# Performance work log

Measured on AMD Instinct MI355X. Metric: run time of the kernel, lower is better.

## Reference

```python
import jax, jax.numpy as jnp
import numpy as np

STATE_DIM = 13
HIDDEN = 1024
NUM_SENSORS = 32
BATCH = 131072


def _sensor_locations():
    # Replicates the torch buffer construction (linspace over theta/phi on a sphere of radius 2)
    sensor_range = 2.0
    theta = np.linspace(0.0, 2.0 * np.pi, NUM_SENSORS // 2, dtype=np.float64)
    phi = np.linspace(0.0, np.pi, 2, dtype=np.float64)
    sensors = []
    for p in phi:
        for t in theta:
            sensors.append([sensor_range * np.sin(p) * np.cos(t),
                            sensor_range * np.sin(p) * np.sin(t),
                            sensor_range * np.cos(p)])
    return jnp.asarray(np.asarray(sensors[:NUM_SENSORS], dtype=np.float32))


def setup_inputs() -> dict:
    key = jax.random.key(0)
    ks = jax.random.split(key, 24)

    def lin(kw, fan_in, fan_out):
        # torch nn.Linear default init: U(-1/sqrt(fan_in), 1/sqrt(fan_in))
        bound = 1.0 / np.sqrt(fan_in)
        w = jax.random.uniform(kw, (fan_in, fan_out), jnp.float32, -bound, bound)
        return w

    def bias(kb, fan_in, fan_out):
        bound = 1.0 / np.sqrt(fan_in)
        return jax.random.uniform(kb, (fan_out,), jnp.float32, -bound, bound)

    branch_in = NUM_SENSORS * (STATE_DIM + 4)  # 544
    h2, h4, h8 = HIDDEN // 2, HIDDEN // 4, HIDDEN // 8
    inp = {
        "state": jax.random.normal(ks[0], (BATCH, STATE_DIM), jnp.float32),
        "action": jax.random.normal(ks[1], (BATCH, 4), jnp.float32),
        "sensor_locations": _sensor_locations(),
        "bw1": lin(ks[2], branch_in, HIDDEN), "bb1": bias(ks[3], branch_in, HIDDEN),
        "bw2": lin(ks[4], HIDDEN, h2), "bb2": bias(ks[5], HIDDEN, h2),
        "bw3": lin(ks[6], h2, h4), "bb3": bias(ks[7], h2, h4),
        "tw1": lin(ks[8], 3, h4), "tb1": bias(ks[9], 3, h4),
        "tw2": lin(ks[10], h4, h4), "tb2": bias(ks[11], h4, h4),
        "qw1": lin(ks[12], 3, h8), "qb1": bias(ks[13], 3, h8),
        "qw2": lin(ks[14], h8, STATE_DIM), "qb2": bias(ks[15], h8, STATE_DIM),
        "pw": lin(ks[16], h4, STATE_DIM), "pb": bias(ks[17], h4, STATE_DIM),
        "residual_weight": jnp.float32(0.1),
    }
    return inp


def reference(state, action, sensor_locations,
              bw1, bb1, bw2, bb2, bw3, bb3,
              tw1, tb1, tw2, tb2,
              qw1, qb1, qw2, qb2,
              pw, pb, residual_weight):
    B = state.shape[0]
    pos = state[:, :3]

    # Vectorized sensor encoding (replaces the 32-iteration python loop):
    # distance [B, S, 1], weight = exp(-d/0.5)
    diff = sensor_locations[None, :, :] - pos[:, None, :]          # [B, S, 3]
    dist = jnp.linalg.norm(diff, axis=-1, keepdims=True)           # [B, S, 1]
    w = jnp.exp(-dist / 0.5)                                       # [B, S, 1]
    sv = jnp.concatenate([state[:, None, :] * w,
                          action[:, None, :] * w], axis=-1)        # [B, S, sd+4]
    enc = sv.reshape(B, -1)                                        # [B, S*(sd+4)]

    # Branch net (dropout is identity in eval mode)
    h = jax.nn.relu(enc @ bw1 + bb1)
    h = jax.nn.relu(h @ bw2 + bb2)
    branch = h @ bw3 + bb3                                         # [B, hidden//4]

    # Trunk net on eval coords
    t = jnp.tanh(pos @ tw1 + tb1)
    trunk = jnp.tanh(t @ tw2 + tb2)                                # [B, hidden//4]

    interaction = branch * trunk
    output_delta = interaction @ pw + pb                           # [B, state_dim]

    b = jax.nn.relu(pos @ qw1 + qb1)
    bias_out = b @ qw2 + qb2                                       # [B, state_dim]

    next_state = state + residual_weight * (output_delta + bias_out)

    # Quaternion normalization for dims 3:7 (state_dim >= 7)
    quat = next_state[:, 3:7]
    qn = jnp.linalg.norm(quat, axis=1, keepdims=True)
    next_state = next_state.at[:, 3:7].set(quat / (qn + 1e-8))
    return next_state
```

## Files before the change

kernel.cpp:

```cpp
#include <hip/hip_runtime.h>
#include <hip/hip_bf16.h>
#include <hip/hip_fp8.h>

#define B_TOTAL 131072

typedef __attribute__((ext_vector_type(8))) short short8;
typedef __attribute__((ext_vector_type(4))) float f32x4;
typedef __attribute__((ext_vector_type(16))) unsigned char uchar16;
typedef unsigned int uint;

#define MFMA(a,b,c) __builtin_amdgcn_mfma_f32_16x16x32_bf16(a,b,c,0,0,0)
#define MFMA8(a,b,c) __builtin_amdgcn_mfma_f32_16x16x32_fp8_fp8(a,b,c,0,0,0)

__device__ __forceinline__ short f2bf(float f) {
  union { float f; uint u; } x; x.f = f;
  uint r = x.u + 0x7fffu + ((x.u >> 16) & 1u);
  return (short)(r >> 16);
}
__device__ __forceinline__ unsigned char f2fp8(float v) {
  union { __hip_fp8_e4m3 q; unsigned char b; } u;
  u.q = __hip_fp8_e4m3(v);
  return u.b;
}
__device__ __forceinline__ float ftanh(float x) {
  float e = __builtin_amdgcn_exp2f(x * 2.8853900817779268f);
  return 1.f - 2.f * __builtin_amdgcn_rcpf(e + 1.f);
}

__device__ __forceinline__ void gl_lds16(const void* g, void* l) {
  __builtin_amdgcn_global_load_lds((const __attribute__((address_space(1))) uint*)g,
                                   (__attribute__((address_space(3))) uint*)l, 16, 0, 0);
}
__device__ __forceinline__ int swz8(int c, int r) { return (c & ~7) | ((c ^ r) & 7); }

__global__ __launch_bounds__(256)
void prep(const float* __restrict__ bw1, const float* __restrict__ bw2,
          const float* __restrict__ bw3, const float* __restrict__ tw2,
          const float* __restrict__ pw, const float* __restrict__ qw2,
          unsigned char* __restrict__ w1f, unsigned char* __restrict__ w2f,
          unsigned char* __restrict__ w3r, short* __restrict__ w4r,
          short* __restrict__ pwT, short* __restrict__ qw2T) {
  __shared__ float tile[32][33];
  int b = blockIdx.x;
  if (b == 1280) {
    for (int t = threadIdx.x; t < 6144; t += 256) {
      if (t < 4096) { int c = t >> 8, k = t & 255;
        pwT[t] = (c < 13) ? f2bf(pw[k * 13 + c]) : (short)0; }
      else { int i = t - 4096; int c = i >> 7, j = i & 127;
        qw2T[i] = (c < 13) ? f2bf(qw2[j * 13 + c]) : (short)0; }
    }
    return;
  }
  const float* src; int K, N, mat;
  if (b < 576)       { src = bw1; K = 544;  N = 1024; mat = 0; }
  else if (b < 1088) { b -= 576;  src = bw2; K = 1024; N = 512;  mat = 1; }
  else if (b < 1216) { b -= 1088; src = bw3; K = 512;  N = 256;  mat = 2; }
  else               { b -= 1216; src = tw2; K = 256;  N = 256;  mat = 3; }
  const int ntk = (mat == 0) ? 18 : (mat == 1) ? 32 : (mat == 2) ? 16 : 8;
  const int tn = b / ntk, tk = b % ntk;
  const int k0 = tk * 32, n0 = tn * 32;
  const int tx = threadIdx.x & 31, ty = threadIdx.x >> 5;
#pragma unroll
  for (int rr = 0; rr < 32; rr += 8) {
    int k = k0 + ty + rr;
    tile[ty + rr][tx] = (k < K) ? src[(long)k * N + n0 + tx] : 0.f;
  }
  __syncthreads();
#pragma unroll
  for (int rr = 0; rr < 32; rr += 8) {
    int nl = ty + rr;
    int n = n0 + nl, k = k0 + tx;
    float v = tile[tx][nl];
    if (mat == 0) w1f[(long)n * 576 + k] = f2fp8(v);
    else if (mat == 1) w2f[(long)n * 1024 + k] = f2fp8(v);
    else {
      int ks = k >> 5, fq = (k >> 3) & 3, j = k & 7;
      int wb = n >> 5, hf = (n >> 4) & 1, fr = n & 15;
      long idx = (long)(((ks * 8 + wb) * 2 + hf) * 4 + fq) * 128 + fr * 8 + j;
      if (mat == 2) w3r[idx] = f2fp8(v);
      else          w4r[idx] = f2bf(v);
    }
  }
}

__global__ __launch_bounds__(256)
void enc_k(const float* __restrict__ state, const float* __restrict__ action,
           const float* __restrict__ sensors, unsigned char* __restrict__ enc) {
  __shared__ float sval[64][17];
  __shared__ float wexp[64][32];
  __shared__ float sens[96];
  const int tid = threadIdx.x;
  const int rb = blockIdx.x * 64;
  if (tid < 96) sens[tid] = sensors[tid];
  for (int i = tid; i < 64 * 17; i += 256) {
    const int r = i / 17, c = i % 17;
    const long grow = rb + r;
    sval[r][c] = (c < 13) ? state[grow * 13 + c] : action[grow * 4 + (c - 13)];
  }
  __syncthreads();
  for (int i = tid; i < 64 * 32; i += 256) {
    const int r = i >> 5, s = i & 31;
    const float dx = sens[s*3+0] - sval[r][0];
    const float dy = sens[s*3+1] - sval[r][1];
    const float dz = sens[s*3+2] - sval[r][2];
    wexp[r][s] = __expf(-2.0f * sqrtf(dx*dx + dy*dy + dz*dz));
  }
  __syncthreads();
  for (int i = tid; i < 64 * 36; i += 256) {
    const int r = i / 36, c16 = i % 36;
    uchar16 v;
#pragma unroll
    for (int j = 0; j < 16; ++j) {
      const int k = c16 * 16 + j;
      unsigned char o = 0;
      if (k < 544) { const int s = k / 17, c = k % 17; o = f2fp8(sval[r][c] * wexp[r][s]); }
      v[j] = o;
    }
    *(uchar16*)&enc[((long)(rb + r)) * 576 + c16 * 16] = v;
  }
}

template<int N, int K, int ACT>
__global__ __launch_bounds__(256, 4)
void gemm_f8(const unsigned char* __restrict__ A, const unsigned char* __restrict__ Bt,
             const float* __restrict__ bias, unsigned char* __restrict__ C) {
  constexpr int NT = K / 64;
  constexpr int NTN = N / 128;
  __shared__ __align__(16) unsigned char As[2][128 * 64];
  __shared__ __align__(16) unsigned char Bs[2][128 * 64];
  const int tid = threadIdx.x;
  const int wave = tid >> 6;
  const int lane = tid & 63;
  const int Mtiles = gridDim.x / NTN;
  const int bid = blockIdx.x;
  const int xcd = bid & 7, seq = bid >> 3;
  const int tm = xcd * (Mtiles >> 3) + seq / NTN;
  const int tn = seq % NTN;
  const long arow0 = (long)tm * 128;
  const long brow0 = (long)tn * 128;

  auto stage = [&](int b, int kt) {
    const int k0 = kt * 64;
#pragma unroll
    for (int it = 0; it < 2; ++it) {
      const int ch = it * 256 + tid;
      const int row = ch >> 2;
      const int cs = (ch & 3) ^ ((row >> 1) & 3);
      gl_lds16(A + (arow0 + row) * (long)K + k0 + cs * 16, &As[b][ch * 16]);
      gl_lds16(Bt + (brow0 + row) * (long)K + k0 + cs * 16, &Bs[b][ch * 16]);
    }
  };

  const int wr = (wave >> 1) * 64;
  const int wc = (wave & 1) * 64;
  const int fr = lane & 15;
  const int fg = lane >> 4;

  f32x4 acc[4][4] = {};

  stage(0, 0);
  for (int kt = 0; kt < NT; ++kt) {
    const int cur = kt & 1;
    __syncthreads();
    if (kt + 1 < NT) stage(cur ^ 1, kt + 1);
    const unsigned char* Ab = As[cur];
    const unsigned char* Bb = Bs[cur];
    long long af[4][2], bfr[4][2];
#pragma unroll
    for (int m = 0; m < 4; ++m)
#pragma unroll
      for (int kk = 0; kk < 2; ++kk) {
        const int row = wr + m * 16 + fr;
        const int c16 = (kk * 2 + (fg >> 1)) ^ ((row >> 1) & 3);
        af[m][kk] = *(const long long*)&Ab[row * 64 + c16 * 16 + (fg & 1) * 8];
      }
#pragma unroll
    for (int n = 0; n < 4; ++n)
#pragma unroll
      for (int kk = 0; kk < 2; ++kk) {
        const int col = wc + n * 16 + fr;
        const int c16 = (kk * 2 + (fg >> 1)) ^ ((col >> 1) & 3);
        bfr[n][kk] = *(const long long*)&Bb[col * 64 + c16 * 16 + (fg & 1) * 8];
      }
#pragma unroll
    for (int kk = 0; kk < 2; ++kk)
#pragma unroll
      for (int m = 0; m < 4; ++m)
#pragma unroll
        for (int n = 0; n < 4; ++n)
          acc[m][n] = MFMA8(af[m][kk], bfr[n][kk], acc[m][n]);
  }

  float bv[4];
#pragma unroll
  for (int n = 0; n < 4; ++n) bv[n] = bias[tn * 128 + wc + n * 16 + fr];
#pragma unroll
  for (int m = 0; m < 4; ++m)
#pragma unroll
    for (int n = 0; n < 4; ++n) {
      const long col = brow0 + wc + n * 16 + fr;
#pragma unroll
      for (int r = 0; r < 4; ++r) {
        const long row = arow0 + wr + m * 16 + fg * 4 + r;
        float v = acc[m][n][r] + bv[n];
        if (ACT == 1) v = fmaxf(v, 0.f);
        C[row * (long)N + col] = f2fp8(v);
      }
    }
}

__global__ __launch_bounds__(512)
void k2(const unsigned char* __restrict__ h2, const float* __restrict__ state,
        const float* __restrict__ tw1, const float* __restrict__ tb1,
        const unsigned char* __restrict__ w3r, const float* __restrict__ bb3,
        const short* __restrict__ w4r, const float* __restrict__ tb2,
        const short* __restrict__ pwT, const float* __restrict__ qw1,
        const short* __restrict__ qw2T, const float* __restrict__ qb1,
        const float* __restrict__ pb, const float* __restrict__ qb2,
        const float* __restrict__ rwp, float* __restrict__ out) {
  __shared__ __align__(16) char lds[77824];
  char*  h2S = lds;
  short* tS  = (short*)(lds + 32768);
  short* pwS = (short*)(lds + 65536);
  short* q2S = (short*)(lds + 73728);
  short* hqS = (short*)lds;
  float* prS = (float*)(lds + 16384);
  float* pr2S= (float*)(lds + 20480);

  const int tid = threadIdx.x, wave = tid >> 6, lane = tid & 63;
  const int fr = lane & 15, fg = lane >> 4;
  const long rb = (long)blockIdx.x * 64;

  long long b3r[16][2];
#pragma unroll
  for (int ks = 0; ks < 16; ++ks) {
    b3r[ks][0] = *(const long long*)&w3r[(long)((ks * 8 + wave) * 2 + 0) * 512 + lane * 8];
    b3r[ks][1] = *(const long long*)&w3r[(long)((ks * 8 + wave) * 2 + 1) * 512 + lane * 8];
  }
#pragma unroll
  for (int it = 0; it < 4; ++it) {
    int ch = it * 512 + tid;
    int row = ch >> 5, c = ch & 31;
    gl_lds16(h2 + (rb + row) * 512 + ((c ^ (row & 7)) << 4), h2S + ch * 16);
  }
  { int row = tid >> 5, c = tid & 31;
    gl_lds16(pwT + (long)row * 256 + swz8(c, row) * 8, (char*)pwS + tid * 16); }
  if (tid < 256) { int row = tid >> 4, c = tid & 15;
    gl_lds16(qw2T + (long)row * 128 + swz8(c, row) * 8, (char*)q2S + tid * 16); }
  short8 b4r[8][2];
#pragma unroll
  for (int ks = 0; ks < 8; ++ks) {
    b4r[ks][0] = *(const short8*)&w4r[(long)((ks * 8 + wave) * 2 + 0) * 512 + lane * 8];
    b4r[ks][1] = *(const short8*)&w4r[(long)((ks * 8 + wave) * 2 + 1) * 512 + lane * 8];
  }

  for (int i = tid; i < 64 * 32; i += 512) {
    int r = i >> 5, c8 = i & 31;
    float p0 = state[(rb + r) * 13 + 0], p1 = state[(rb + r) * 13 + 1], p2 = state[(rb + r) * 13 + 2];
    short8 v;
#pragma unroll
    for (int j = 0; j < 8; ++j) {
      int jj = c8 * 8 + j;
      v[j] = f2bf(ftanh(p0 * tw1[jj] + p1 * tw1[256 + jj] + p2 * tw1[512 + jj] + tb1[jj]));
    }
    *(short8*)&tS[(r * 32 + swz8(c8, r)) * 8] = v;
  }
  __syncthreads();

  f32x4 acc3[4][2] = {};
#pragma unroll
  for (int ks = 0; ks < 16; ++ks) {
    long long a[4];
#pragma unroll
    for (int mf = 0; mf < 4; ++mf) {
      int row = mf * 16 + fr;
      int c16 = (ks * 2 + (fg >> 1)) ^ (row & 7);
      a[mf] = *(const long long*)&h2S[row * 512 + c16 * 16 + ((fg & 1) << 3)];
    }
#pragma unroll
    for (int mf = 0; mf < 4; ++mf) {
      acc3[mf][0] = MFMA8(a[mf], b3r[ks][0], acc3[mf][0]);
      acc3[mf][1] = MFMA8(a[mf], b3r[ks][1], acc3[mf][1]);
    }
  }

  f32x4 accT[4][2] = {};
#pragma unroll
  for (int ks = 0; ks < 8; ++ks) {
#pragma unroll
    for (int mf = 0; mf < 4; ++mf) {
      int row = mf * 16 + fr;
      short8 aF = *(const short8*)&tS[row * 256 + swz8(ks * 4 + fg, row) * 8];
      accT[mf][0] = MFMA(aF, b4r[ks][0], accT[mf][0]);
      accT[mf][1] = MFMA(aF, b4r[ks][1], accT[mf][1]);
    }
  }
  __syncthreads();

#pragma unroll
  for (int nf = 0; nf < 2; ++nf) {
    int col = wave * 32 + nf * 16 + fr;
    float b3 = bb3[col], t2 = tb2[col];
#pragma unroll
    for (int mf = 0; mf < 4; ++mf)
#pragma unroll
      for (int i = 0; i < 4; ++i) {
        int row = mf * 16 + fg * 4 + i;
        float br = acc3[mf][nf][i] + b3;
        float tr = ftanh(accT[mf][nf][i] + t2);
        tS[row * 256 + swz8(col >> 3, row) * 8 + (col & 7)] = f2bf(br * tr);
      }
  }
  {
    int r = tid >> 3, j0 = (tid & 7) * 16;
    float p0 = state[(rb + r) * 13 + 0], p1 = state[(rb + r) * 13 + 1], p2 = state[(rb + r) * 13 + 2];
#pragma unroll
    for (int cc = 0; cc < 2; ++cc) {
      short8 v;
#pragma unroll
      for (int j = 0; j < 8; ++j) {
        int jj = j0 + cc * 8 + j;
        float hv = fmaxf(p0 * qw1[jj] + p1 * qw1[128 + jj] + p2 * qw1[256 + jj] + qb1[jj], 0.f);
        v[j] = f2bf(hv);
      }
      *(short8*)&hqS[(r * 16 + swz8(j0 / 8 + cc, r)) * 8] = v;
    }
  }
  __syncthreads();

  if (wave < 4) {
    int row = wave * 16 + fr;
    f32x4 accP = {0.f, 0.f, 0.f, 0.f};
#pragma unroll
    for (int ks = 0; ks < 8; ++ks) {
      short8 a = *(const short8*)&tS[row * 256 + swz8(ks * 4 + fg, row) * 8];
      short8 b = *(const short8*)&pwS[fr * 256 + swz8(ks * 4 + fg, fr) * 8];
      accP = MFMA(a, b, accP);
    }
#pragma unroll
    for (int i = 0; i < 4; ++i)
      prS[(wave * 16 + fg * 4 + i) * 16 + fr] = accP[i];
  } else {
    int row = (wave - 4) * 16 + fr;
    f32x4 accQ = {0.f, 0.f, 0.f, 0.f};
#pragma unroll
    for (int ks = 0; ks < 4; ++ks) {
      short8 a = *(const short8*)&hqS[row * 128 + swz8(ks * 4 + fg, row) * 8];
      short8 b = *(const short8*)&q2S[fr * 128 + swz8(ks * 4 + fg, fr) * 8];
      accQ = MFMA(a, b, accQ);
    }
#pragma unroll
    for (int i = 0; i < 4; ++i)
      pr2S[((wave - 4) * 16 + fg * 4 + i) * 16 + fr] = accQ[i];
  }
  __syncthreads();

  if (tid < 64) {
    int r = tid;
    float rw = rwp[0];
    float ns[13];
#pragma unroll
    for (int c = 0; c < 13; ++c)
      ns[c] = state[(rb + r) * 13 + c] + rw * (prS[r * 16 + c] + pr2S[r * 16 + c] + pb[c] + qb2[c]);
    float qn = sqrtf(ns[3] * ns[3] + ns[4] * ns[4] + ns[5] * ns[5] + ns[6] * ns[6]) + 1e-8f;
#pragma unroll
    for (int c = 3; c < 7; ++c) ns[c] /= qn;
#pragma unroll
    for (int c = 0; c < 13; ++c) out[(rb + r) * 13 + c] = ns[c];
  }
}

extern "C" void kernel_launch(void* const* d_in, const int* in_sizes, int n_in,
                              void* d_out, int out_size, void* d_ws, size_t ws_size,
                              hipStream_t stream) {
  const float* state  = (const float*)d_in[0];
  const float* action = (const float*)d_in[1];
  const float* sensors= (const float*)d_in[2];
  const float* bw1 = (const float*)d_in[3];
  const float* bb1 = (const float*)d_in[4];
  const float* bw2 = (const float*)d_in[5];
  const float* bb2 = (const float*)d_in[6];
  const float* bw3 = (const float*)d_in[7];
  const float* bb3 = (const float*)d_in[8];
  const float* tw1 = (const float*)d_in[9];
  const float* tb1 = (const float*)d_in[10];
  const float* tw2 = (const float*)d_in[11];
  const float* tb2 = (const float*)d_in[12];
  const float* qw1 = (const float*)d_in[13];
  const float* qb1 = (const float*)d_in[14];
  const float* qw2 = (const float*)d_in[15];
  const float* qb2 = (const float*)d_in[16];
  const float* pw  = (const float*)d_in[17];
  const float* pb  = (const float*)d_in[18];
  const float* rw  = (const float*)d_in[19];
  float* out = (float*)d_out;

  char* p = (char*)d_ws;
  unsigned char* w1f = (unsigned char*)p; p += (size_t)1024 * 576;
  unsigned char* w2f = (unsigned char*)p; p += (size_t)512 * 1024;
  unsigned char* w3r = (unsigned char*)p; p += (size_t)256 * 512;
  short* w4r = (short*)p;          p += (size_t)256 * 256 * 2;
  short* pwT = (short*)p;          p += (size_t)16 * 256 * 2;
  short* qw2T= (short*)p;          p += (size_t)16 * 128 * 2;
  const size_t fixed = (size_t)(p - (char*)d_ws);
  const size_t avail = (ws_size > fixed) ? ws_size - fixed : 0;
  long Mc = (long)(avail / 1600) & ~1023L;
  if (Mc > B_TOTAL) Mc = B_TOTAL;
  if (Mc < 1024) return;
  unsigned char* encb = (unsigned char*)p;
  unsigned char* h2b  = (unsigned char*)p;
  unsigned char* h1f  = (unsigned char*)(p + (size_t)Mc * 576);

  prep<<<dim3(1281), dim3(256), 0, stream>>>(bw1, bw2, bw3, tw2, pw, qw2,
                                             w1f, w2f, w3r, w4r, pwT, qw2T);

  for (long r0 = 0; r0 < B_TOTAL; r0 += Mc) {
    long Mr = B_TOTAL - r0; if (Mr > Mc) Mr = Mc;
    enc_k<<<dim3(Mr / 64), dim3(256), 0, stream>>>(state + r0 * 13, action + r0 * 4,
                                                   sensors, encb);
    gemm_f8<1024, 576, 1><<<dim3((Mr / 128) * 8), dim3(256), 0, stream>>>(
        encb, w1f, bb1, h1f);
    gemm_f8<512, 1024, 1><<<dim3((Mr / 128) * 4), dim3(256), 0, stream>>>(
        h1f, w2f, bb2, h2b);
    k2<<<dim3(Mr / 64), dim3(512), 0, stream>>>(h2b, state + r0 * 13, tw1, tb1,
                                                w3r, bb3, w4r, tb2, pwT, qw1, qw2T,
                                                qb1, pb, qb2, rw, out + r0 * 13);
  }
}
```

Measured before the change: 376.1 us.

## Permute K layout so fp8 GEMM fragments load as single 16-byte LDS reads

Reorders the K dimension of the encoded input, the fp8 weight matrices and the intermediate activations with a fixed permutation. Each lane can then fetch both K-halves of its MFMA fragment with one 128-bit LDS load instead of two 64-bit loads. The GEMM epilogue writes permuted columns, and the downstream k2 reader is adjusted to match. This cuts the number of LDS read instructions in the inner loop, at the cost of a more intricate layout contract shared by several kernels.

```diff
diff --git a/kernel.cpp b/kernel.cpp
--- a/kernel.cpp
+++ b/kernel.cpp
@@ -7,6 +7,7 @@
 typedef __attribute__((ext_vector_type(8))) short short8;
 typedef __attribute__((ext_vector_type(4))) float f32x4;
 typedef __attribute__((ext_vector_type(16))) unsigned char uchar16;
+typedef __attribute__((ext_vector_type(2))) long long llong2;
 typedef unsigned int uint;
 
 #define MFMA(a,b,c) __builtin_amdgcn_mfma_f32_16x16x32_bf16(a,b,c,0,0,0)
@@ -32,6 +33,10 @@
                                    (__attribute__((address_space(3))) uint*)l, 16, 0, 0);
 }
 __device__ __forceinline__ int swz8(int c, int r) { return (c & ~7) | ((c ^ r) & 7); }
+
+__device__ __forceinline__ int permk(int k) {
+  return (k & ~63) | (((k >> 3) & 3) << 4) | (((k >> 5) & 1) << 3) | (k & 7);
+}
 
 __global__ __launch_bounds__(256)
 void prep(const float* __restrict__ bw1, const float* __restrict__ bw2,
@@ -71,8 +76,8 @@
     int nl = ty + rr;
     int n = n0 + nl, k = k0 + tx;
     float v = tile[tx][nl];
-    if (mat == 0) w1f[(long)n * 576 + k] = f2fp8(v);
-    else if (mat == 1) w2f[(long)n * 1024 + k] = f2fp8(v);
+    if (mat == 0) w1f[(long)n * 576 + permk(k)] = f2fp8(v);
+    else if (mat == 1) w2f[(long)n * 1024 + permk(k)] = f2fp8(v);
     else {
       int ks = k >> 5, fq = (k >> 3) & 3, j = k & 7;
       int wb = n >> 5, hf = (n >> 4) & 1, fr = n & 15;
@@ -110,11 +115,13 @@
     const int r = i / 36, c16 = i % 36;
     uchar16 v;
 #pragma unroll
-    for (int j = 0; j < 16; ++j) {
-      const int k = c16 * 16 + j;
+    for (int j2 = 0; j2 < 16; ++j2) {
+      const int soff = c16 * 16 + j2;
+      const int kb = soff >> 6, bb = soff & 63;
+      const int k = kb * 64 + ((bb >> 3) & 1) * 32 + (bb >> 4) * 8 + (bb & 7);
       unsigned char o = 0;
       if (k < 544) { const int s = k / 17, c = k % 17; o = f2fp8(sval[r][c] * wexp[r][s]); }
-      v[j] = o;
+      v[j2] = o;
     }
     *(uchar16*)&enc[((long)(rb + r)) * 576 + c16 * 16] = v;
   }
@@ -165,30 +172,27 @@
     if (kt + 1 < NT) stage(cur ^ 1, kt + 1);
     const unsigned char* Ab = As[cur];
     const unsigned char* Bb = Bs[cur];
-    long long af[4][2], bfr[4][2];
+    llong2 av[4], bv2[4];
+#pragma unroll
+    for (int m = 0; m < 4; ++m) {
+      const int row = wr + m * 16 + fr;
+      av[m] = *(const llong2*)&Ab[row * 64 + ((fg ^ ((row >> 1) & 3)) << 4)];
+    }
+#pragma unroll
+    for (int n = 0; n < 4; ++n) {
+      const int col = wc + n * 16 + fr;
+      bv2[n] = *(const llong2*)&Bb[col * 64 + ((fg ^ ((col >> 1) & 3)) << 4)];
+    }
 #pragma unroll
     for (int m = 0; m < 4; ++m)
 #pragma unroll
-      for (int kk = 0; kk < 2; ++kk) {
-        const int row = wr + m * 16 + fr;
-        const int c16 = (kk * 2 + (fg >> 1)) ^ ((row >> 1) & 3);
-        af[m][kk] = *(const long long*)&Ab[row * 64 + c16 * 16 + (fg & 1) * 8];
-      }
-#pragma unroll
-    for (int n = 0; n < 4; ++n)
-#pragma unroll
-      for (int kk = 0; kk < 2; ++kk) {
-        const int col = wc + n * 16 + fr;
-        const int c16 = (kk * 2 + (fg >> 1)) ^ ((col >> 1) & 3);
-        bfr[n][kk] = *(const long long*)&Bb[col * 64 + c16 * 16 + (fg & 1) * 8];
-      }
-#pragma unroll
-    for (int kk = 0; kk < 2; ++kk)
-#pragma unroll
-      for (int m = 0; m < 4; ++m)
-#pragma unroll
-        for (int n = 0; n < 4; ++n)
-          acc[m][n] = MFMA8(af[m][kk], bfr[n][kk], acc[m][n]);
+      for (int n = 0; n < 4; ++n)
+        acc[m][n] = MFMA8(av[m][0], bv2[n][0], acc[m][n]);
+#pragma unroll
+    for (int m = 0; m < 4; ++m)
+#pragma unroll
+      for (int n = 0; n < 4; ++n)
+        acc[m][n] = MFMA8(av[m][1], bv2[n][1], acc[m][n]);
   }
 
   float bv[4];
@@ -198,7 +202,8 @@
   for (int m = 0; m < 4; ++m)
 #pragma unroll
     for (int n = 0; n < 4; ++n) {
-      const long col = brow0 + wc + n * 16 + fr;
+      const int colp = permk(tn * 128 + wc + n * 16 + fr);
+      const long col = (long)colp;
 #pragma unroll
       for (int r = 0; r < 4; ++r) {
         const long row = arow0 + wr + m * 16 + fg * 4 + r;
@@ -274,8 +279,8 @@
 #pragma unroll
     for (int mf = 0; mf < 4; ++mf) {
       int row = mf * 16 + fr;
-      int c16 = (ks * 2 + (fg >> 1)) ^ (row & 7);
-      a[mf] = *(const long long*)&h2S[row * 512 + c16 * 16 + ((fg & 1) << 3)];
+      int c16 = ((ks >> 1) * 4 + fg) ^ (row & 7);
+      a[mf] = *(const long long*)&h2S[row * 512 + (c16 << 4) + ((ks & 1) << 3)];
     }
 #pragma unroll
     for (int mf = 0; mf < 4; ++mf) {
```

New measurement: 381.8 us. About the same (+1.5%).

## Switch branch GEMMs to scaled 16x16x128 FP8 MFMA with K-tile 128

Applied to the files above, without the earlier changes.

Replaces the two fp8 branch-net GEMMs' 16x16x32 MFMAs with the MX scaled 16x16x128 f8f6f4 instruction using unit scales, doubling the LDS K-tile to 128 with a new 8-way swizzle. The first layer's K is padded from 576 to 640 so it divides by 128, which changes the encoder and weight-prep layouts and the workspace sizing. The aim is fewer MFMA issues and higher matrix throughput. In exchange, LDS use doubles, occupancy is lowered to 2 blocks per CU, and layer 1 does extra padded work.

```diff
diff --git a/kernel.cpp b/kernel.cpp
--- a/kernel.cpp
+++ b/kernel.cpp
@@ -7,10 +7,16 @@
 typedef __attribute__((ext_vector_type(8))) short short8;
 typedef __attribute__((ext_vector_type(4))) float f32x4;
 typedef __attribute__((ext_vector_type(16))) unsigned char uchar16;
+typedef __attribute__((ext_vector_type(4))) int int4v;
+typedef __attribute__((ext_vector_type(8))) int int8v;
 typedef unsigned int uint;
 
 #define MFMA(a,b,c) __builtin_amdgcn_mfma_f32_16x16x32_bf16(a,b,c,0,0,0)
 #define MFMA8(a,b,c) __builtin_amdgcn_mfma_f32_16x16x32_fp8_fp8(a,b,c,0,0,0)
+#define MFMAS(a,b,c) __builtin_amdgcn_mfma_scale_f32_16x16x128_f8f6f4( \
+    a, b, c, 0, 0, 0, 0x7F7F7F7F, 0, 0x7F7F7F7F)
+
+union V8U { int8v v; int4v h[2]; };
 
 __device__ __forceinline__ short f2bf(float f) {
   union { float f; uint u; } x; x.f = f;
@@ -42,7 +48,7 @@
           short* __restrict__ pwT, short* __restrict__ qw2T) {
   __shared__ float tile[32][33];
   int b = blockIdx.x;
-  if (b == 1280) {
+  if (b == 1344) {
     for (int t = threadIdx.x; t < 6144; t += 256) {
       if (t < 4096) { int c = t >> 8, k = t & 255;
         pwT[t] = (c < 13) ? f2bf(pw[k * 13 + c]) : (short)0; }
@@ -52,11 +58,11 @@
     return;
   }
   const float* src; int K, N, mat;
-  if (b < 576)       { src = bw1; K = 544;  N = 1024; mat = 0; }
-  else if (b < 1088) { b -= 576;  src = bw2; K = 1024; N = 512;  mat = 1; }
-  else if (b < 1216) { b -= 1088; src = bw3; K = 512;  N = 256;  mat = 2; }
-  else               { b -= 1216; src = tw2; K = 256;  N = 256;  mat = 3; }
-  const int ntk = (mat == 0) ? 18 : (mat == 1) ? 32 : (mat == 2) ? 16 : 8;
+  if (b < 640)       { src = bw1; K = 544;  N = 1024; mat = 0; }
+  else if (b < 1152) { b -= 640;  src = bw2; K = 1024; N = 512;  mat = 1; }
+  else if (b < 1280) { b -= 1152; src = bw3; K = 512;  N = 256;  mat = 2; }
+  else               { b -= 1280; src = tw2; K = 256;  N = 256;  mat = 3; }
+  const int ntk = (mat == 0) ? 20 : (mat == 1) ? 32 : (mat == 2) ? 16 : 8;
   const int tn = b / ntk, tk = b % ntk;
   const int k0 = tk * 32, n0 = tn * 32;
   const int tx = threadIdx.x & 31, ty = threadIdx.x >> 5;
@@ -71,7 +77,7 @@
     int nl = ty + rr;
     int n = n0 + nl, k = k0 + tx;
     float v = tile[tx][nl];
-    if (mat == 0) w1f[(long)n * 576 + k] = f2fp8(v);
+    if (mat == 0) w1f[(long)n * 640 + k] = f2fp8(v);
     else if (mat == 1) w2f[(long)n * 1024 + k] = f2fp8(v);
     else {
       int ks = k >> 5, fq = (k >> 3) & 3, j = k & 7;
@@ -106,8 +112,8 @@
     wexp[r][s] = __expf(-2.0f * sqrtf(dx*dx + dy*dy + dz*dz));
   }
   __syncthreads();
-  for (int i = tid; i < 64 * 36; i += 256) {
-    const int r = i / 36, c16 = i % 36;
+  for (int i = tid; i < 64 * 40; i += 256) {
+    const int r = i / 40, c16 = i % 40;
     uchar16 v;
 #pragma unroll
     for (int j = 0; j < 16; ++j) {
@@ -116,18 +122,18 @@
       if (k < 544) { const int s = k / 17, c = k % 17; o = f2fp8(sval[r][c] * wexp[r][s]); }
       v[j] = o;
     }
-    *(uchar16*)&enc[((long)(rb + r)) * 576 + c16 * 16] = v;
+    *(uchar16*)&enc[((long)(rb + r)) * 640 + c16 * 16] = v;
   }
 }
 
 template<int N, int K, int ACT>
-__global__ __launch_bounds__(256, 4)
-void gemm_f8(const unsigned char* __restrict__ A, const unsigned char* __restrict__ Bt,
+__global__ __launch_bounds__(256, 2)
+void gemm_mx(const unsigned char* __restrict__ A, const unsigned char* __restrict__ Bt,
              const float* __restrict__ bias, unsigned char* __restrict__ C) {
-  constexpr int NT = K / 64;
+  constexpr int NT = K / 128;
   constexpr int NTN = N / 128;
-  __shared__ __align__(16) unsigned char As[2][128 * 64];
-  __shared__ __align__(16) unsigned char Bs[2][128 * 64];
+  __shared__ __align__(16) unsigned char As[2][128 * 128];
+  __shared__ __align__(16) unsigned char Bs[2][128 * 128];
   const int tid = threadIdx.x;
   const int wave = tid >> 6;
   const int lane = tid & 63;
@@ -140,12 +146,12 @@
   const long brow0 = (long)tn * 128;
 
   auto stage = [&](int b, int kt) {
-    const int k0 = kt * 64;
-#pragma unroll
-    for (int it = 0; it < 2; ++it) {
+    const int k0 = kt * 128;
+#pragma unroll
+    for (int it = 0; it < 4; ++it) {
       const int ch = it * 256 + tid;
-      const int row = ch >> 2;
-      const int cs = (ch & 3) ^ ((row >> 1) & 3);
+      const int row = ch >> 3;
+      const int cs = (ch & 7) ^ (row & 7);
       gl_lds16(A + (arow0 + row) * (long)K + k0 + cs * 16, &As[b][ch * 16]);
       gl_lds16(Bt + (brow0 + row) * (long)K + k0 + cs * 16, &Bs[b][ch * 16]);
     }
@@ -165,30 +171,30 @@
     if (kt + 1 < NT) stage(cur ^ 1, kt + 1);
     const unsigned char* Ab = As[cur];
     const unsigned char* Bb = Bs[cur];
-    long long af[4][2], bfr[4][2];
+    int8v av[4], bv2[4];
+#pragma unroll
+    for (int m = 0; m < 4; ++m) {
+      const int row = wr + m * 16 + fr;
+      const int p0 = (2 * fg) ^ (row & 7);
+      V8U u;
+      u.h[0] = *(const int4v*)&Ab[row * 128 + (p0 << 4)];
+      u.h[1] = *(const int4v*)&Ab[row * 128 + ((p0 ^ 1) << 4)];
+      av[m] = u.v;
+    }
+#pragma unroll
+    for (int n = 0; n < 4; ++n) {
+      const int col = wc + n * 16 + fr;
+      const int p0 = (2 * fg) ^ (col & 7);
+      V8U u;
+      u.h[0] = *(const int4v*)&Bb[col * 128 + (p0 << 4)];
+      u.h[1] = *(const int4v*)&Bb[col * 128 + ((p0 ^ 1) << 4)];
+      bv2[n] = u.v;
+    }
 #pragma unroll
     for (int m = 0; m < 4; ++m)
 #pragma unroll
-      for (int kk = 0; kk < 2; ++kk) {
-        const int row = wr + m * 16 + fr;
-        const int c16 = (kk * 2 + (fg >> 1)) ^ ((row >> 1) & 3);
-        af[m][kk] = *(const long long*)&Ab[row * 64 + c16 * 16 + (fg & 1) * 8];
-      }
-#pragma unroll
-    for (int n = 0; n < 4; ++n)
-#pragma unroll
-      for (int kk = 0; kk < 2; ++kk) {
-        const int col = wc + n * 16 + fr;
-        const int c16 = (kk * 2 + (fg >> 1)) ^ ((col >> 1) & 3);
-        bfr[n][kk] = *(const long long*)&Bb[col * 64 + c16 * 16 + (fg & 1) * 8];
-      }
-#pragma unroll
-    for (int kk = 0; kk < 2; ++kk)
-#pragma unroll
-      for (int m = 0; m < 4; ++m)
-#pragma unroll
-        for (int n = 0; n < 4; ++n)
-          acc[m][n] = MFMA8(af[m][kk], bfr[n][kk], acc[m][n]);
+      for (int n = 0; n < 4; ++n)
+        acc[m][n] = MFMAS(av[m], bv2[n], acc[m][n]);
   }
 
   float bv[4];
@@ -275,7 +281,7 @@
     for (int mf = 0; mf < 4; ++mf) {
       int row = mf * 16 + fr;
       int c16 = (ks * 2 + (fg >> 1)) ^ (row & 7);
-      a[mf] = *(const long long*)&h2S[row * 512 + c16 * 16 + ((fg & 1) << 3)];
+      a[mf] = *(const long long*)&h2S[row * 512 + (c16 << 4) + ((fg & 1) << 3)];
     }
 #pragma unroll
     for (int mf = 0; mf < 4; ++mf) {
@@ -396,7 +402,7 @@
   float* out = (float*)d_out;
 
   char* p = (char*)d_ws;
-  unsigned char* w1f = (unsigned char*)p; p += (size_t)1024 * 576;
+  unsigned char* w1f = (unsigned char*)p; p += (size_t)1024 * 640;
   unsigned char* w2f = (unsigned char*)p; p += (size_t)512 * 1024;
   unsigned char* w3r = (unsigned char*)p; p += (size_t)256 * 512;
   short* w4r = (short*)p;          p += (size_t)256 * 256 * 2;
@@ -404,23 +410,23 @@
   short* qw2T= (short*)p;          p += (size_t)16 * 128 * 2;
   const size_t fixed = (size_t)(p - (char*)d_ws);
   const size_t avail = (ws_size > fixed) ? ws_size - fixed : 0;
-  long Mc = (long)(avail / 1600) & ~1023L;
+  long Mc = (long)(avail / 1664) & ~1023L;
   if (Mc > B_TOTAL) Mc = B_TOTAL;
   if (Mc < 1024) return;
   unsigned char* encb = (unsigned char*)p;
   unsigned char* h2b  = (unsigned char*)p;
-  unsigned char* h1f  = (unsigned char*)(p + (size_t)Mc * 576);
-
-  prep<<<dim3(1281), dim3(256), 0, stream>>>(bw1, bw2, bw3, tw2, pw, qw2,
+  unsigned char* h1f  = (unsigned char*)(p + (size_t)Mc * 640);
+
+  prep<<<dim3(1345), dim3(256), 0, stream>>>(bw1, bw2, bw3, tw2, pw, qw2,
                                              w1f, w2f, w3r, w4r, pwT, qw2T);
 
   for (long r0 = 0; r0 < B_TOTAL; r0 += Mc) {
     long Mr = B_TOTAL - r0; if (Mr > Mc) Mr = Mc;
     enc_k<<<dim3(Mr / 64), dim3(256), 0, stream>>>(state + r0 * 13, action + r0 * 4,
                                                    sensors, encb);
-    gemm_f8<1024, 576, 1><<<dim3((Mr / 128) * 8), dim3(256), 0, stream>>>(
+    gemm_mx<1024, 640, 1><<<dim3((Mr / 128) * 8), dim3(256), 0, stream>>>(
         encb, w1f, bb1, h1f);
-    gemm_f8<512, 1024, 1><<<dim3((Mr / 128) * 4), dim3(256), 0, stream>>>(
+    gemm_mx<512, 1024, 1><<<dim3((Mr / 128) * 4), dim3(256), 0, stream>>>(
         h1f, w2f, bb2, h2b);
     k2<<<dim3(Mr / 64), dim3(512), 0, stream>>>(h2b, state + r0 * 13, tw1, tb1,
                                                 w3r, bb3, w4r, tb2, pwT, qw1, qw2T,
```

New measurement: 365.7 us. 1.03x faster.
